# Kernel tuning notes

Hardware: AMD Instinct MI355X
Metric: run time of the kernel (lower is better)

Reference implementation:

```python
import jax, jax.numpy as jnp
import numpy as np

N, F, H, C, E = 20000, 512, 128, 64, 640000


def _uniform(key, shape, stdv):
    return jax.random.uniform(key, shape, jnp.float32, -stdv, stdv)


def setup_inputs() -> dict:
    key = jax.random.key(0)
    ks = jax.random.split(key, 20)
    inp = {}
    for i, name in enumerate(['x1', 'x2', 'x3']):
        inp[name] = jax.random.normal(ks[i], (N, F), jnp.float32)
    for v, base in zip([1, 2, 3], [3, 6, 9]):
        inp[f'src{v}'] = jax.random.randint(ks[base], (E,), 0, N, jnp.int32)
        inp[f'dst{v}'] = jax.random.randint(ks[base + 1], (E,), 0, N, jnp.int32)
        inp[f'val{v}'] = jax.random.uniform(ks[base + 2], (E,), jnp.float32)
    s1 = 1.0 / np.sqrt(H)
    s2 = 1.0 / np.sqrt(C)
    sv = 1.0 / np.sqrt(3.0)
    inp['W1'] = _uniform(ks[12], (3, 3, F, H), s1)   # [gc, view_role, F, H]
    inp['wv1'] = _uniform(ks[13], (3, 3), sv)
    inp['b1'] = _uniform(ks[14], (3, H), sv)
    inp['W2'] = _uniform(ks[15], (3, 3, H, C), s2)
    inp['wv2'] = _uniform(ks[16], (3, 3), sv)
    inp['b2'] = _uniform(ks[17], (3, C), sv)
    return inp


def _spmm(src, dst, val, emb, n):
    # out[i] = sum_{edges e with src=i} val[e] * emb[dst[e]]
    return jax.ops.segment_sum(val[:, None] * emb[dst], src, num_segments=n)


def _igc(xs, adjs, W, wv, b, n):
    # xs: [x_self, x_v2, x_v3]; adjs: matching [(src,dst,val)]*3
    embs = [xs[i] @ W[i] for i in range(3)]
    neigh = [_spmm(adjs[i][0], adjs[i][1], adjs[i][2], embs[i], n) for i in range(3)]
    agg = wv[0] * neigh[0] + wv[1] * neigh[1] + wv[2] * neigh[2]
    return embs[0] + 1.01 * agg + b


def reference(x1, x2, x3, src1, dst1, val1, src2, dst2, val2, src3, dst3, val3,
              W1, wv1, b1, W2, wv2, b2):
    n = x1.shape[0]
    a1, a2, a3 = (src1, dst1, val1), (src2, dst2, val2), (src3, dst3, val3)
    relu = jax.nn.relu
    h1 = relu(_igc([x1, x2, x3], [a1, a2, a3], W1[0], wv1[0], b1[0], n))
    h2 = relu(_igc([x2, x1, x3], [a2, a1, a3], W1[1], wv1[1], b1[1], n))
    h3 = relu(_igc([x3, x1, x2], [a3, a1, a2], W1[2], wv1[2], b1[2], n))
    y1 = relu(_igc([h1, h2, h3], [a1, a2, a3], W2[0], wv2[0], b2[0], n))
    y2 = relu(_igc([h2, h1, h3], [a2, a1, a3], W2[1], wv2[1], b2[1], n))
    y3 = relu(_igc([h3, h1, h2], [a3, a1, a2], W2[2], wv2[2], b2[2], n))
    return jnp.abs((y1 + y2 + y3) / 3.0)
```

## Files before the change

kernel.cpp:

```cpp
#include <hip/hip_runtime.h>
#include <hip/hip_bf16.h>

#define N_NODES 20000
#define F_DIM   512
#define H_DIM   128
#define C_DIM   64
#define E_EDGES 640000

#define P_WV1   64
#define P_B1    80
#define P_WV2   464
#define P_B2    480
#define P_E     1024
#define P_H     (P_E + 3*N_NODES*H_DIM)
#define P_YSUM  (P_H + 3*N_NODES*H_DIM)
#define RP_SZ      20032
#define CSR_STRIDE (RP_SZ + 2*E_EDGES)
#define P_CSR   (P_YSUM + N_NODES*C_DIM)
#define P_CUR   (P_CSR + 3*CSR_STRIDE)
#define P_WT1   (P_E + 4000000)
#define P_WT2   (P_E + 4300000)
#define P_W1H   (P_YSUM)
#define P_W1L   (P_YSUM + 294912)
#define P_W2H   (P_E + 4000000)
#define P_W2L   (P_E + 4050000)
#define NBUCK       8
#define BUCK_SHIFT  12
#define B2_STRIDE   (N_NODES * NBUCK)
#define NBLK_SCAN   625
#define BSUM_STRIDE 640

typedef __attribute__((ext_vector_type(8))) unsigned short u16x8;
typedef __attribute__((ext_vector_type(8))) __bf16 bf16x8;
typedef __attribute__((ext_vector_type(4))) float f32x4;

__device__ inline float cvt(float x) { return x; }
__device__ inline float cvt(__hip_bfloat16 x) { return __bfloat162float(x); }

__device__ inline void store_out(float v, float* p) { *p = v; }
__device__ inline void store_out(float v, __hip_bfloat16* p) { *p = __float2bfloat16(v); }

__device__ inline unsigned short f2bf_bits(float x) {
    __hip_bfloat16 b = __float2bfloat16(x);
    return *(unsigned short*)&b;
}
__device__ inline void splitbf(float x, unsigned short& h, unsigned short& l) {
    h = f2bf_bits(x);
    float hf = __uint_as_float(((unsigned int)h) << 16);
    l = f2bf_bits(x - hf);
}

__global__ void detect_kernel(const unsigned short* __restrict__ x, int* flag) {
    __shared__ int cnt;
    if (threadIdx.x == 0) cnt = 0;
    __syncthreads();
    int c = 0;
    for (int i = threadIdx.x; i < 4096; i += 256) {
        int ex = (x[i] >> 7) & 0xff;
        if (ex >= 140) c++;
    }
    atomicAdd(&cnt, c);
    __syncthreads();
    if (threadIdx.x == 0) *flag = (cnt > 64) ? 1 : 0;
}

__global__ void prep_kernel(const int* __restrict__ flag,
                            const void* wv1, const void* b1,
                            const void* wv2, const void* b2, float* ws) {
    bool f32 = (*flag == 1);
    int t = threadIdx.x;
    auto get = [&](const void* p, int i) -> float {
        return f32 ? ((const float*)p)[i]
                   : __bfloat162float(((const __hip_bfloat16*)p)[i]);
    };
    if (t < 9) ws[P_WV1 + t] = get(wv1, t);
    if (t < 9) ws[P_WV2 + t] = get(wv2, t);
    for (int i = t; i < 3*H_DIM; i += 256) ws[P_B1 + i] = get(b1, i);
    for (int i = t; i < 3*C_DIM; i += 256) ws[P_B2 + i] = get(b2, i);
}

__global__ __launch_bounds__(256)
void hist2_kernel(const int* __restrict__ s0, const int* __restrict__ d0,
                  const int* __restrict__ s1, const int* __restrict__ d1,
                  const int* __restrict__ s2, const int* __restrict__ d2,
                  int* __restrict__ deg2) {
    int e = blockIdx.x * 256 + threadIdx.x;
    if (e >= E_EDGES) return;
    const int z = blockIdx.y;
    const int* src = (z == 0) ? s0 : (z == 1) ? s1 : s2;
    const int* dst = (z == 0) ? d0 : (z == 1) ? d1 : d2;
    int idx = src[e] * NBUCK + (dst[e] >> BUCK_SHIFT);
    atomicAdd(&deg2[z * B2_STRIDE + idx], 1);
}

__global__ __launch_bounds__(256)
void scanA_kernel(int* __restrict__ deg2, int* __restrict__ bsum) {
    __shared__ int s[256];
    const int z = blockIdx.y;
    int* d = deg2 + z * B2_STRIDE;
    const int t = threadIdx.x;
    const int i = blockIdx.x * 256 + t;
    int v = d[i];
    s[t] = v;
    __syncthreads();
    for (int off = 1; off < 256; off <<= 1) {
        int u = (t >= off) ? s[t - off] : 0;
        __syncthreads();
        s[t] += u;
        __syncthreads();
    }
    d[i] = s[t] - v;
    if (t == 255) bsum[z * BSUM_STRIDE + blockIdx.x] = s[255];
}

__global__ __launch_bounds__(256)
void scanB_kernel(int* __restrict__ bsum) {
    __shared__ int sums[256];
    int* b = bsum + blockIdx.x * BSUM_STRIDE;
    const int t = threadIdx.x;
    int beg = t * 3, end = beg + 3; if (end > NBLK_SCAN) end = NBLK_SCAN;
    int s = 0;
    for (int i = beg; i < end && i < NBLK_SCAN; ++i) s += b[i];
    sums[t] = s;
    __syncthreads();
    for (int off = 1; off < 256; off <<= 1) {
        int u = (t >= off) ? sums[t - off] : 0;
        __syncthreads();
        sums[t] += u;
        __syncthreads();
    }
    int run = sums[t] - s;
    for (int i = beg; i < end && i < NBLK_SCAN; ++i) { int v = b[i]; b[i] = run; run += v; }
}

__global__ __launch_bounds__(256)
void scanC_kernel(int* __restrict__ deg2, const int* __restrict__ bsum,
                  int* __restrict__ rpBase) {
    const int z = blockIdx.y;
    int* d = deg2 + z * B2_STRIDE;
    int* rowptr = rpBase + (long)z * CSR_STRIDE;
    const int i = blockIdx.x * 256 + threadIdx.x;
    int v = d[i] + bsum[z * BSUM_STRIDE + blockIdx.x];
    d[i] = v;
    if ((i & (NBUCK - 1)) == 0) rowptr[i >> 3] = v;
    if (i == 0) rowptr[N_NODES] = E_EDGES;
}

__global__ __launch_bounds__(256)
void fill3_kernel(const int* __restrict__ flag,
                  const int* __restrict__ s0, const int* __restrict__ d0,
                  const void* __restrict__ v0,
                  const int* __restrict__ s1, const int* __restrict__ d1,
                  const void* __restrict__ v1,
                  const int* __restrict__ s2, const int* __restrict__ d2,
                  const void* __restrict__ v2,
                  const int* __restrict__ deg2, int* __restrict__ cur2,
                  int* __restrict__ rpBase) {
    int e = blockIdx.x * 256 + threadIdx.x;
    if (e >= E_EDGES) return;
    const int z = blockIdx.y;
    const int* src = (z == 0) ? s0 : (z == 1) ? s1 : s2;
    const int* dst = (z == 0) ? d0 : (z == 1) ? d1 : d2;
    const void* val = (z == 0) ? v0 : (z == 1) ? v1 : v2;
    float v = (*flag == 1) ? ((const float*)val)[e]
                           : __bfloat162float(((const __hip_bfloat16*)val)[e]);
    int d = dst[e];
    int idx = z * B2_STRIDE + src[e] * NBUCK + (d >> BUCK_SHIFT);
    int pos = deg2[idx] + atomicAdd(&cur2[idx], 1);
    int2* ed = (int2*)(rpBase + (long)z * CSR_STRIDE + RP_SZ);
    ed[pos] = make_int2(d, __float_as_int(v));
}

__global__ __launch_bounds__(256)
void transpose_w_kernel(const int* __restrict__ flag,
                        const void* __restrict__ Wsrc,
                        unsigned short* __restrict__ Wt, int K, int HO) {
    if (*flag != 0) return;
    __shared__ unsigned short T[64][80];
    const unsigned short* W = (const unsigned short*)Wsrc + (long)blockIdx.z * K * HO;
    unsigned short* O = Wt + (long)blockIdx.z * HO * K;
    const int k0 = blockIdx.x * 64, n0 = blockIdx.y * 64;
    const int t = threadIdx.x;
    const int rr = t >> 3, cc = (t & 7) * 8;
    #pragma unroll
    for (int i = 0; i < 2; ++i) {
        int k = rr + i * 32;
        *(u16x8*)&T[k][cc] = *(const u16x8*)&W[(long)(k0 + k) * HO + n0 + cc];
    }
    __syncthreads();
    #pragma unroll
    for (int i = 0; i < 2; ++i) {
        int nn = rr + i * 32;
        u16x8 v;
        #pragma unroll
        for (int j = 0; j < 8; ++j) v[j] = T[cc + j][nn];
        *(u16x8*)&O[(long)(n0 + nn) * K + k0 + cc] = v;
    }
}

__global__ __launch_bounds__(256)
void split_w_kernel(const int* __restrict__ flag,
                    const float* __restrict__ Wsrc,
                    unsigned short* __restrict__ Wh,
                    unsigned short* __restrict__ Wl, int K, int HO) {
    if (*flag != 1) return;
    __shared__ float T[64][68];
    const float* W = Wsrc + (long)blockIdx.z * K * HO;
    unsigned short* Oh = Wh + (long)blockIdx.z * HO * K;
    unsigned short* Ol = Wl + (long)blockIdx.z * HO * K;
    const int k0 = blockIdx.x * 64, n0 = blockIdx.y * 64;
    const int t = threadIdx.x;
    #pragma unroll
    for (int i = 0; i < 16; ++i) {
        int idx = t + i * 256;
        int r = idx >> 6, c = idx & 63;
        T[r][c] = W[(long)(k0 + r) * HO + n0 + c];
    }
    __syncthreads();
    #pragma unroll
    for (int i = 0; i < 16; ++i) {
        int idx = t + i * 256;
        int nn = idx >> 6, kk = idx & 63;
        unsigned short h, l;
        splitbf(T[kk][nn], h, l);
        Oh[(long)(n0 + nn) * K + k0 + kk] = h;
        Ol[(long)(n0 + nn) * K + k0 + kk] = l;
    }
}

#define SWZ(r, kb) (((r) << 7) + ((kb) ^ (((r) & 7) << 4)))

__global__ __launch_bounds__(256)
void gemm_mfma1_kernel(const int* __restrict__ flag,
                       const unsigned short* __restrict__ x0,
                       const unsigned short* __restrict__ x1,
                       const unsigned short* __restrict__ x2,
                       const unsigned short* __restrict__ WtBase,
                       unsigned short* __restrict__ outBase, int n) {
    if (*flag != 0) return;
    const int role = blockIdx.y;
    const unsigned short* X = (role == 0) ? x0 : (role == 1) ? x1 : x2;
    const unsigned short* Wt = WtBase + (long)role * H_DIM * F_DIM;
    unsigned short* out = outBase + (long)role * N_NODES * H_DIM;
    __shared__ __align__(16) unsigned short As[64 * 64];
    __shared__ __align__(16) unsigned short Bs[128 * 64];
    const int t = threadIdx.x;
    const int lane = t & 63;
    const int wave = t >> 6;
    const int wm = wave & 1, wn = wave >> 1;
    const int row0 = blockIdx.x * 64;
    const int rl = lane & 15;
    const int kq = lane >> 4;
    const int sr = t >> 3;
    const int sc = (t & 7) * 8;
    f32x4 acc[2][4] = {};
    for (int k0 = 0; k0 < F_DIM; k0 += 64) {
        #pragma unroll
        for (int i = 0; i < 2; ++i) {
            int r = i * 32 + sr;
            int gr = row0 + r; if (gr >= n) gr = n - 1;
            u16x8 v = *(const u16x8*)&X[(long)gr * F_DIM + k0 + sc];
            *(u16x8*)((char*)As + SWZ(r, sc * 2)) = v;
        }
        #pragma unroll
        for (int i = 0; i < 4; ++i) {
            int r = i * 32 + sr;
            u16x8 v = *(const u16x8*)&Wt[(long)r * F_DIM + k0 + sc];
            *(u16x8*)((char*)Bs + SWZ(r, sc * 2)) = v;
        }
        __syncthreads();
        #pragma unroll
        for (int s = 0; s < 2; ++s) {
            const int kb = s * 64 + kq * 16;
            bf16x8 af[2], bfr[4];
            #pragma unroll
            for (int mi = 0; mi < 2; ++mi) {
                int r = wm * 32 + mi * 16 + rl;
                af[mi] = *(const bf16x8*)((const char*)As + SWZ(r, kb));
            }
            #pragma unroll
            for (int ni = 0; ni < 4; ++ni) {
                int r = wn * 64 + ni * 16 + rl;
                bfr[ni] = *(const bf16x8*)((const char*)Bs + SWZ(r, kb));
            }
            #pragma unroll
            for (int mi = 0; mi < 2; ++mi)
                #pragma unroll
                for (int ni = 0; ni < 4; ++ni)
                    acc[mi][ni] = __builtin_amdgcn_mfma_f32_16x16x32_bf16(
                        af[mi], bfr[ni], acc[mi][ni], 0, 0, 0);
        }
        __syncthreads();
    }
    #pragma unroll
    for (int mi = 0; mi < 2; ++mi) {
        #pragma unroll
        for (int q = 0; q < 4; ++q) {
            int row = row0 + wm * 32 + mi * 16 + kq * 4 + q;
            if (row < n) {
                #pragma unroll
                for (int ni = 0; ni < 4; ++ni) {
                    int col = wn * 64 + ni * 16 + rl;
                    out[(long)row * H_DIM + col] = f2bf_bits(acc[mi][ni][q]);
                }
            }
        }
    }
}

__global__ __launch_bounds__(256)
void gemm_mfma1f_kernel(const int* __restrict__ flag,
                        const float* __restrict__ x0,
                        const float* __restrict__ x1,
                        const float* __restrict__ x2,
                        const unsigned short* __restrict__ WhBase,
                        const unsigned short* __restrict__ WlBase,
                        float* __restrict__ outBase, int n) {
    if (*flag != 1) return;
    const int role = blockIdx.y;
    const float* X = (role == 0) ? x0 : (role == 1) ? x1 : x2;
    const unsigned short* Wh = WhBase + (long)role * H_DIM * F_DIM;
    const unsigned short* Wl = WlBase + (long)role * H_DIM * F_DIM;
    float* out = outBase + (long)role * N_NODES * H_DIM;
    __shared__ __align__(16) unsigned short Ash[64 * 64];
    __shared__ __align__(16) unsigned short Asl[64 * 64];
    __shared__ __align__(16) unsigned short Bsh[128 * 64];
    __shared__ __align__(16) unsigned short Bsl[128 * 64];
    const int t = threadIdx.x;
    const int lane = t & 63;
    const int wave = t >> 6;
    const int wm = wave & 1, wn = wave >> 1;
    const int row0 = blockIdx.x * 64;
    const int rl = lane & 15;
    const int kq = lane >> 4;
    const int sr = t >> 3;
    const int sc = (t & 7) * 8;
    f32x4 acc[2][4] = {};
    for (int k0 = 0; k0 < F_DIM; k0 += 64) {
        #pragma unroll
        for (int i = 0; i < 2; ++i) {
            int r = i * 32 + sr;
            int gr = row0 + r; if (gr >= n) gr = n - 1;
            float4 v0 = *(const float4*)&X[(long)gr * F_DIM + k0 + sc];
            float4 v1 = *(const float4*)&X[(long)gr * F_DIM + k0 + sc + 4];
            float xs[8] = {v0.x, v0.y, v0.z, v0.w, v1.x, v1.y, v1.z, v1.w};
            u16x8 hi, lo;
            #pragma unroll
            for (int j = 0; j < 8; ++j) { unsigned short h, l; splitbf(xs[j], h, l); hi[j] = h; lo[j] = l; }
            *(u16x8*)((char*)Ash + SWZ(r, sc * 2)) = hi;
            *(u16x8*)((char*)Asl + SWZ(r, sc * 2)) = lo;
        }
        #pragma unroll
        for (int i = 0; i < 4; ++i) {
            int r = i * 32 + sr;
            u16x8 vh = *(const u16x8*)&Wh[(long)r * F_DIM + k0 + sc];
            u16x8 vl = *(const u16x8*)&Wl[(long)r * F_DIM + k0 + sc];
            *(u16x8*)((char*)Bsh + SWZ(r, sc * 2)) = vh;
            *(u16x8*)((char*)Bsl + SWZ(r, sc * 2)) = vl;
        }
        __syncthreads();
        #pragma unroll
        for (int s = 0; s < 2; ++s) {
            const int kb = s * 64 + kq * 16;
            bf16x8 ah[2], al[2], bh[4], bl[4];
            #pragma unroll
            for (int mi = 0; mi < 2; ++mi) {
                int r = wm * 32 + mi * 16 + rl;
                ah[mi] = *(const bf16x8*)((const char*)Ash + SWZ(r, kb));
                al[mi] = *(const bf16x8*)((const char*)Asl + SWZ(r, kb));
            }
            #pragma unroll
            for (int ni = 0; ni < 4; ++ni) {
                int r = wn * 64 + ni * 16 + rl;
                bh[ni] = *(const bf16x8*)((const char*)Bsh + SWZ(r, kb));
                bl[ni] = *(const bf16x8*)((const char*)Bsl + SWZ(r, kb));
            }
            #pragma unroll
            for (int mi = 0; mi < 2; ++mi)
                #pragma unroll
                for (int ni = 0; ni < 4; ++ni) {
                    acc[mi][ni] = __builtin_amdgcn_mfma_f32_16x16x32_bf16(
                        ah[mi], bh[ni], acc[mi][ni], 0, 0, 0);
                    acc[mi][ni] = __builtin_amdgcn_mfma_f32_16x16x32_bf16(
                        ah[mi], bl[ni], acc[mi][ni], 0, 0, 0);
                    acc[mi][ni] = __builtin_amdgcn_mfma_f32_16x16x32_bf16(
                        al[mi], bh[ni], acc[mi][ni], 0, 0, 0);
                }
        }
        __syncthreads();
    }
    #pragma unroll
    for (int mi = 0; mi < 2; ++mi) {
        #pragma unroll
        for (int q = 0; q < 4; ++q) {
            int row = row0 + wm * 32 + mi * 16 + kq * 4 + q;
            if (row < n) {
                #pragma unroll
                for (int ni = 0; ni < 4; ++ni) {
                    int col = wn * 64 + ni * 16 + rl;
                    out[(long)row * H_DIM + col] = acc[mi][ni][q];
                }
            }
        }
    }
}

#define SWZ2(r, kb) (((r) << 8) + ((kb) ^ (((r) & 7) << 4)))

__global__ __launch_bounds__(256)
void gemm_mfma2_kernel(const int* __restrict__ flag,
                       const unsigned short* __restrict__ h0,
                       const unsigned short* __restrict__ h1,
                       const unsigned short* __restrict__ h2,
                       const unsigned short* __restrict__ WtBase,
                       unsigned short* __restrict__ outBase, int n) {
    if (*flag != 0) return;
    const int role = blockIdx.y;
    const unsigned short* X = (role == 0) ? h0 : (role == 1) ? h1 : h2;
    const unsigned short* Wt = WtBase + (long)role * C_DIM * H_DIM;
    unsigned short* out = outBase + (long)role * N_NODES * C_DIM;
    __shared__ __align__(16) unsigned short As[64 * 128];
    __shared__ __align__(16) unsigned short Bs[64 * 128];
    const int t = threadIdx.x;
    const int lane = t & 63;
    const int wave = t >> 6;
    const int wm = wave & 1, wn = wave >> 1;
    const int row0 = blockIdx.x * 64;
    const int rl = lane & 15;
    const int kq = lane >> 4;
    #pragma unroll
    for (int i = 0; i < 4; ++i) {
        int e = t + i * 256;
        int r = e >> 4, c8 = e & 15;
        int gr = row0 + r; if (gr >= n) gr = n - 1;
        u16x8 va = *(const u16x8*)&X[(long)gr * H_DIM + c8 * 8];
        *(u16x8*)((char*)As + SWZ2(r, c8 * 16)) = va;
        u16x8 vb = *(const u16x8*)&Wt[(long)r * H_DIM + c8 * 8];
        *(u16x8*)((char*)Bs + SWZ2(r, c8 * 16)) = vb;
    }
    __syncthreads();
    f32x4 acc[2][2] = {};
    #pragma unroll
    for (int s = 0; s < 4; ++s) {
        const int kb = s * 64 + kq * 16;
        bf16x8 af[2], bfr[2];
        #pragma unroll
        for (int mi = 0; mi < 2; ++mi) {
            int r = wm * 32 + mi * 16 + rl;
            af[mi] = *(const bf16x8*)((const char*)As + SWZ2(r, kb));
        }
        #pragma unroll
        for (int ni = 0; ni < 2; ++ni) {
            int r = wn * 32 + ni * 16 + rl;
            bfr[ni] = *(const bf16x8*)((const char*)Bs + SWZ2(r, kb));
        }
        #pragma unroll
        for (int mi = 0; mi < 2; ++mi)
            #pragma unroll
            for (int ni = 0; ni < 2; ++ni)
                acc[mi][ni] = __builtin_amdgcn_mfma_f32_16x16x32_bf16(
                    af[mi], bfr[ni], acc[mi][ni], 0, 0, 0);
    }
    #pragma unroll
    for (int mi = 0; mi < 2; ++mi) {
        #pragma unroll
        for (int q = 0; q < 4; ++q) {
            int row = row0 + wm * 32 + mi * 16 + kq * 4 + q;
            if (row < n) {
                #pragma unroll
                for (int ni = 0; ni < 2; ++ni) {
                    int col = wn * 32 + ni * 16 + rl;
                    out[(long)row * C_DIM + col] = f2bf_bits(acc[mi][ni][q]);
                }
            }
        }
    }
}

__global__ __launch_bounds__(256)
void gemm_mfma2f_kernel(const int* __restrict__ flag,
                        const float* __restrict__ h0,
                        const float* __restrict__ h1,
                        const float* __restrict__ h2,
                        const unsigned short* __restrict__ WhBase,
                        const unsigned short* __restrict__ WlBase,
                        float* __restrict__ outBase, int n) {
    if (*flag != 1) return;
    const int role = blockIdx.y;
    const float* X = (role == 0) ? h0 : (role == 1) ? h1 : h2;
    const unsigned short* Wh = WhBase + (long)role * C_DIM * H_DIM;
    const unsigned short* Wl = WlBase + (long)role * C_DIM * H_DIM;
    float* out = outBase + (long)role * N_NODES * C_DIM;
    __shared__ __align__(16) unsigned short Ash[64 * 128];
    __shared__ __align__(16) unsigned short Asl[64 * 128];
    __shared__ __align__(16) unsigned short Bsh[64 * 128];
    __shared__ __align__(16) unsigned short Bsl[64 * 128];
    const int t = threadIdx.x;
    const int lane = t & 63;
    const int wave = t >> 6;
    const int wm = wave & 1, wn = wave >> 1;
    const int row0 = blockIdx.x * 64;
    const int rl = lane & 15;
    const int kq = lane >> 4;
    #pragma unroll
    for (int i = 0; i < 4; ++i) {
        int e = t + i * 256;
        int r = e >> 4, c8 = e & 15;
        int gr = row0 + r; if (gr >= n) gr = n - 1;
        float4 v0 = *(const float4*)&X[(long)gr * H_DIM + c8 * 8];
        float4 v1 = *(const float4*)&X[(long)gr * H_DIM + c8 * 8 + 4];
        float xs[8] = {v0.x, v0.y, v0.z, v0.w, v1.x, v1.y, v1.z, v1.w};
        u16x8 hi, lo;
        #pragma unroll
        for (int j = 0; j < 8; ++j) { unsigned short h, l; splitbf(xs[j], h, l); hi[j] = h; lo[j] = l; }
        *(u16x8*)((char*)Ash + SWZ2(r, c8 * 16)) = hi;
        *(u16x8*)((char*)Asl + SWZ2(r, c8 * 16)) = lo;
        u16x8 vh = *(const u16x8*)&Wh[(long)r * H_DIM + c8 * 8];
        u16x8 vl = *(const u16x8*)&Wl[(long)r * H_DIM + c8 * 8];
        *(u16x8*)((char*)Bsh + SWZ2(r, c8 * 16)) = vh;
        *(u16x8*)((char*)Bsl + SWZ2(r, c8 * 16)) = vl;
    }
    __syncthreads();
    f32x4 acc[2][2] = {};
    #pragma unroll
    for (int s = 0; s < 4; ++s) {
        const int kb = s * 64 + kq * 16;
        bf16x8 ah[2], al[2], bh[2], bl[2];
        #pragma unroll
        for (int mi = 0; mi < 2; ++mi) {
            int r = wm * 32 + mi * 16 + rl;
            ah[mi] = *(const bf16x8*)((const char*)Ash + SWZ2(r, kb));
            al[mi] = *(const bf16x8*)((const char*)Asl + SWZ2(r, kb));
        }
        #pragma unroll
        for (int ni = 0; ni < 2; ++ni) {
            int r = wn * 32 + ni * 16 + rl;
            bh[ni] = *(const bf16x8*)((const char*)Bsh + SWZ2(r, kb));
            bl[ni] = *(const bf16x8*)((const char*)Bsl + SWZ2(r, kb));
        }
        #pragma unroll
        for (int mi = 0; mi < 2; ++mi)
            #pragma unroll
            for (int ni = 0; ni < 2; ++ni) {
                acc[mi][ni] = __builtin_amdgcn_mfma_f32_16x16x32_bf16(
                    ah[mi], bh[ni], acc[mi][ni], 0, 0, 0);
                acc[mi][ni] = __builtin_amdgcn_mfma_f32_16x16x32_bf16(
                    ah[mi], bl[ni], acc[mi][ni], 0, 0, 0);
                acc[mi][ni] = __builtin_amdgcn_mfma_f32_16x16x32_bf16(
                    al[mi], bh[ni], acc[mi][ni], 0, 0, 0);
            }
    }
    #pragma unroll
    for (int mi = 0; mi < 2; ++mi) {
        #pragma unroll
        for (int q = 0; q < 4; ++q) {
            int row = row0 + wm * 32 + mi * 16 + kq * 4 + q;
            if (row < n) {
                #pragma unroll
                for (int ni = 0; ni < 2; ++ni) {
                    int col = wn * 32 + ni * 16 + rl;
                    out[(long)row * C_DIM + col] = acc[mi][ni][q];
                }
            }
        }
    }
}

template <int FP, bool ACCUM>
__global__ __launch_bounds__(256)
void spmm_f32_kernel(const int* __restrict__ flag,
                     const int* __restrict__ rp0, const int2* __restrict__ ed0,
                     const int* __restrict__ rp1, const int2* __restrict__ ed1,
                     const int* __restrict__ rp2, const int2* __restrict__ ed2,
                     const float* __restrict__ Et0, const float* __restrict__ Et1,
                     const float* __restrict__ Et2,
                     const float* __restrict__ wvp, const float* __restrict__ bias,
                     float* __restrict__ out) {
    if (*flag != 1) return;
    constexpr int HO = FP * 64;
    const int node = blockIdx.x * 4 + (threadIdx.x >> 6);
    const int lane = threadIdx.x & 63;
    const int fbase = lane * FP;
    float acc[FP];
    #pragma unroll
    for (int k = 0; k < FP; ++k) acc[k] = 0.f;

    const int*  rps[3] = {rp0, rp1, rp2};
    const int2* eds[3] = {ed0, ed1, ed2};
    const float* Ets[3] = {Et0, Et1, Et2};
    #pragma unroll
    for (int r = 0; r < 3; ++r) {
        const float s = 1.01f * wvp[r];
        const int2* ed = eds[r];
        const float* Et = Ets[r] + fbase;
        int e = rps[r][node];
        const int end = rps[r][node + 1];
        for (; e + 8 <= end; e += 8) {
            int2 E[8]; float vv[8]; const float* rr[8];
            #pragma unroll
            for (int q = 0; q < 8; ++q) E[q] = ed[e + q];
            #pragma unroll
            for (int q = 0; q < 8; ++q) {
                vv[q] = s * __int_as_float(E[q].y);
                rr[q] = Et + (long)E[q].x * HO;
            }
            #pragma unroll
            for (int q = 0; q < 8; ++q)
                #pragma unroll
                for (int k = 0; k < FP; ++k) acc[k] += vv[q] * rr[q][k];
        }
        for (; e + 2 <= end; e += 2) {
            int2 E0 = ed[e], E1 = ed[e + 1];
            float v0 = s * __int_as_float(E0.y), v1 = s * __int_as_float(E1.y);
            const float* r0 = Et + (long)E0.x * HO;
            const float* r1 = Et + (long)E1.x * HO;
            #pragma unroll
            for (int k = 0; k < FP; ++k) acc[k] += v0 * r0[k];
            #pragma unroll
            for (int k = 0; k < FP; ++k) acc[k] += v1 * r1[k];
        }
        if (e < end) {
            int2 E0 = ed[e];
            float v0 = s * __int_as_float(E0.y);
            const float* r0 = Et + (long)E0.x * HO;
            #pragma unroll
            for (int k = 0; k < FP; ++k) acc[k] += v0 * r0[k];
        }
    }
    const float* e0 = Et0 + (long)node * HO + fbase;
    const float* bp = bias + fbase;
    float* o = out + (long)node * HO + fbase;
    #pragma unroll
    for (int k = 0; k < FP; ++k) {
        float x = e0[k] + acc[k] + bp[k];
        x = x > 0.f ? x : 0.f;
        if (ACCUM) o[k] += x; else o[k] = x;
    }
}

template <int HO, bool ACCUM, bool OUT_BF16>
__global__ __launch_bounds__(256)
void spmm_bf16_kernel(const int* __restrict__ flag,
                      const int* __restrict__ rp0, const int2* __restrict__ ed0,
                      const int* __restrict__ rp1, const int2* __restrict__ ed1,
                      const int* __restrict__ rp2, const int2* __restrict__ ed2,
                      const unsigned short* __restrict__ Et0,
                      const unsigned short* __restrict__ Et1,
                      const unsigned short* __restrict__ Et2,
                      const float* __restrict__ wvp, const float* __restrict__ bias,
                      void* __restrict__ outp) {
    if (*flag != 0) return;
    constexpr int NL = HO / 2;
    constexpr int NPW = 64 / NL;
    const int t = threadIdx.x;
    const int lane = t & 63;
    const int li = lane % NL;
    const int node = blockIdx.x * (4 * NPW) + (t >> 6) * NPW + lane / NL;
    const int fl = li * 2;
    float a0 = 0.f, a1 = 0.f;

    const int*  rps[3] = {rp0, rp1, rp2};
    const int2* eds[3] = {ed0, ed1, ed2};
    const unsigned int* Ets[3] = {(const unsigned int*)Et0,
                                  (const unsigned int*)Et1,
                                  (const unsigned int*)Et2};
    #pragma unroll
    for (int r = 0; r < 3; ++r) {
        const float s = 1.01f * wvp[r];
        const int2* ed = eds[r];
        const unsigned int* Et = Ets[r] + li;
        int e = rps[r][node];
        const int end = rps[r][node + 1];
        for (; e + 4 <= end; e += 4) {
            int2 E0 = ed[e], E1 = ed[e + 1], E2 = ed[e + 2], E3 = ed[e + 3];
            float v0 = s * __int_as_float(E0.y), v1 = s * __int_as_float(E1.y);
            float v2 = s * __int_as_float(E2.y), v3 = s * __int_as_float(E3.y);
            unsigned int w0 = Et[(long)E0.x * NL];
            unsigned int w1 = Et[(long)E1.x * NL];
            unsigned int w2 = Et[(long)E2.x * NL];
            unsigned int w3 = Et[(long)E3.x * NL];
            a0 += v0 * __uint_as_float(w0 << 16);
            a1 += v0 * __uint_as_float(w0 & 0xffff0000u);
            a0 += v1 * __uint_as_float(w1 << 16);
            a1 += v1 * __uint_as_float(w1 & 0xffff0000u);
            a0 += v2 * __uint_as_float(w2 << 16);
            a1 += v2 * __uint_as_float(w2 & 0xffff0000u);
            a0 += v3 * __uint_as_float(w3 << 16);
            a1 += v3 * __uint_as_float(w3 & 0xffff0000u);
        }
        for (; e < end; ++e) {
            int2 E0 = ed[e];
            float v0 = s * __int_as_float(E0.y);
            unsigned int w0 = Et[(long)E0.x * NL];
            a0 += v0 * __uint_as_float(w0 << 16);
            a1 += v0 * __uint_as_float(w0 & 0xffff0000u);
        }
    }
    unsigned int ws0 = ((const unsigned int*)Et0)[(long)node * NL + li];
    float x0 = __uint_as_float(ws0 << 16)        + a0 + bias[fl];
    float x1 = __uint_as_float(ws0 & 0xffff0000u) + a1 + bias[fl + 1];
    x0 = x0 > 0.f ? x0 : 0.f;
    x1 = x1 > 0.f ? x1 : 0.f;
    if (OUT_BF16) {
        unsigned int packed = ((unsigned int)f2bf_bits(x1) << 16) | f2bf_bits(x0);
        ((unsigned int*)outp)[(long)node * NL + li] = packed;
    } else {
        float* o = (float*)outp + (long)node * HO + fl;
        if (ACCUM) { o[0] += x0; o[1] += x1; }
        else       { o[0] = x0;  o[1] = x1; }
    }
}

template <typename TOUT>
__global__ __launch_bounds__(256)
void final_kernel(const int* __restrict__ flag, int want,
                  const float* __restrict__ ysum, TOUT* __restrict__ out, int n) {
    if (*flag != want) return;
    int i = blockIdx.x * 256 + threadIdx.x;
    if (i >= n) return;
    store_out(fabsf(ysum[i] * (1.f / 3.f)), &out[i]);
}

extern "C" void kernel_launch(void* const* d_in, const int* in_sizes, int n_in,
                              void* d_out, int out_size, void* d_ws, size_t ws_size,
                              hipStream_t stream) {
    float* ws = (float*)d_ws;
    int* flag = (int*)d_ws;
    static const int perm[3][3] = {{0, 1, 2}, {1, 0, 2}, {2, 0, 1}};

    detect_kernel<<<1, 256, 0, stream>>>((const unsigned short*)d_in[0], flag);
    prep_kernel<<<1, 256, 0, stream>>>(flag, d_in[13], d_in[14], d_in[16], d_in[17], ws);

    int* csrbase = (int*)(ws + P_CSR);
    int* rp[3]; int2* ed[3];
    for (int j = 0; j < 3; ++j) {
        rp[j] = csrbase + (long)j * CSR_STRIDE;
        ed[j] = (int2*)(rp[j] + RP_SZ);
    }
    {
        int* deg2 = (int*)(ws + P_YSUM);
        int* cur2 = deg2 + 3 * B2_STRIDE;
        int* bsum = cur2 + 3 * B2_STRIDE;
        hipMemsetAsync(deg2, 0, (size_t)6 * B2_STRIDE * 4, stream);
        dim3 ge((E_EDGES + 255) / 256, 3);
        hist2_kernel<<<ge, 256, 0, stream>>>(
            (const int*)d_in[3], (const int*)d_in[4],
            (const int*)d_in[6], (const int*)d_in[7],
            (const int*)d_in[9], (const int*)d_in[10], deg2);
        dim3 gs(NBLK_SCAN, 3);
        scanA_kernel<<<gs, 256, 0, stream>>>(deg2, bsum);
        scanB_kernel<<<3, 256, 0, stream>>>(bsum);
        scanC_kernel<<<gs, 256, 0, stream>>>(deg2, bsum, csrbase);
        fill3_kernel<<<ge, 256, 0, stream>>>(
            flag,
            (const int*)d_in[3], (const int*)d_in[4], d_in[5],
            (const int*)d_in[6], (const int*)d_in[7], d_in[8],
            (const int*)d_in[9], (const int*)d_in[10], d_in[11],
            deg2, cur2, csrbase);
    }

    unsigned short* Wt1 = (unsigned short*)(ws + P_WT1);
    unsigned short* Wt2 = (unsigned short*)(ws + P_WT2);
    {
        dim3 g1(F_DIM / 64, H_DIM / 64, 9);
        transpose_w_kernel<<<g1, 256, 0, stream>>>(flag, d_in[12], Wt1, F_DIM, H_DIM);
        dim3 g2(H_DIM / 64, C_DIM / 64, 9);
        transpose_w_kernel<<<g2, 256, 0, stream>>>(flag, d_in[15], Wt2, H_DIM, C_DIM);
    }
    unsigned short* W1h = (unsigned short*)(ws + P_W1H);
    unsigned short* W1l = (unsigned short*)(ws + P_W1L);
    {
        dim3 g1(F_DIM / 64, H_DIM / 64, 9);
        split_w_kernel<<<g1, 256, 0, stream>>>(flag, (const float*)d_in[12],
                                               W1h, W1l, F_DIM, H_DIM);
    }

    unsigned short* Eb = (unsigned short*)(ws + P_E);
    unsigned short* Hb = (unsigned short*)(ws + P_H);

    const int gemmBlocks = (N_NODES + 63) / 64;

    for (int v = 0; v < 3; ++v) {
        int j0 = perm[v][0], j1 = perm[v][1], j2 = perm[v][2];
        dim3 g(gemmBlocks, 3);
        gemm_mfma1_kernel<<<g, 256, 0, stream>>>(
            flag,
            (const unsigned short*)d_in[j0], (const unsigned short*)d_in[j1],
            (const unsigned short*)d_in[j2],
            Wt1 + (long)v * 3 * H_DIM * F_DIM, Eb, N_NODES);
        gemm_mfma1f_kernel<<<g, 256, 0, stream>>>(
            flag,
            (const float*)d_in[j0], (const float*)d_in[j1], (const float*)d_in[j2],
            W1h + (long)v * 3 * H_DIM * F_DIM, W1l + (long)v * 3 * H_DIM * F_DIM,
            ws + P_E, N_NODES);

        spmm_bf16_kernel<128, false, true><<<N_NODES / 4, 256, 0, stream>>>(
            flag, rp[j0], ed[j0], rp[j1], ed[j1], rp[j2], ed[j2],
            Eb, Eb + (long)N_NODES * H_DIM, Eb + 2L * N_NODES * H_DIM,
            ws + P_WV1 + v * 3, ws + P_B1 + v * H_DIM,
            Hb + (long)v * N_NODES * H_DIM);
        spmm_f32_kernel<2, false><<<N_NODES / 4, 256, 0, stream>>>(
            flag, rp[j0], ed[j0], rp[j1], ed[j1], rp[j2], ed[j2],
            ws + P_E, ws + P_E + (long)N_NODES * H_DIM, ws + P_E + 2L * N_NODES * H_DIM,
            ws + P_WV1 + v * 3, ws + P_B1 + v * H_DIM,
            ws + P_H + (long)v * N_NODES * H_DIM);
    }

    unsigned short* W2h = (unsigned short*)(ws + P_W2H);
    unsigned short* W2l = (unsigned short*)(ws + P_W2L);
    {
        dim3 g2(H_DIM / 64, C_DIM / 64, 9);
        split_w_kernel<<<g2, 256, 0, stream>>>(flag, (const float*)d_in[15],
                                               W2h, W2l, H_DIM, C_DIM);
    }

    for (int v = 0; v < 3; ++v) {
        int j0 = perm[v][0], j1 = perm[v][1], j2 = perm[v][2];
        dim3 g(gemmBlocks, 3);
        gemm_mfma2_kernel<<<g, 256, 0, stream>>>(
            flag,
            Hb + (long)j0 * N_NODES * H_DIM, Hb + (long)j1 * N_NODES * H_DIM,
            Hb + (long)j2 * N_NODES * H_DIM,
            Wt2 + (long)v * 3 * C_DIM * H_DIM, Eb, N_NODES);
        gemm_mfma2f_kernel<<<g, 256, 0, stream>>>(
            flag,
            ws + P_H + (long)j0 * N_NODES * H_DIM,
            ws + P_H + (long)j1 * N_NODES * H_DIM,
            ws + P_H + (long)j2 * N_NODES * H_DIM,
            W2h + (long)v * 3 * C_DIM * H_DIM, W2l + (long)v * 3 * C_DIM * H_DIM,
            ws + P_E, N_NODES);

        if (v == 0) {
            spmm_bf16_kernel<64, false, false><<<N_NODES / 8, 256, 0, stream>>>(
                flag, rp[j0], ed[j0], rp[j1], ed[j1], rp[j2], ed[j2],
                Eb, Eb + (long)N_NODES * C_DIM, Eb + 2L * N_NODES * C_DIM,
                ws + P_WV2 + v * 3, ws + P_B2 + v * C_DIM, ws + P_YSUM);
            spmm_f32_kernel<1, false><<<N_NODES / 4, 256, 0, stream>>>(
                flag, rp[j0], ed[j0], rp[j1], ed[j1], rp[j2], ed[j2],
                ws + P_E, ws + P_E + (long)N_NODES * C_DIM, ws + P_E + 2L * N_NODES * C_DIM,
                ws + P_WV2 + v * 3, ws + P_B2 + v * C_DIM, ws + P_YSUM);
        } else {
            spmm_bf16_kernel<64, true, false><<<N_NODES / 8, 256, 0, stream>>>(
                flag, rp[j0], ed[j0], rp[j1], ed[j1], rp[j2], ed[j2],
                Eb, Eb + (long)N_NODES * C_DIM, Eb + 2L * N_NODES * C_DIM,
                ws + P_WV2 + v * 3, ws + P_B2 + v * C_DIM, ws + P_YSUM);
            spmm_f32_kernel<1, true><<<N_NODES / 4, 256, 0, stream>>>(
                flag, rp[j0], ed[j0], rp[j1], ed[j1], rp[j2], ed[j2],
                ws + P_E, ws + P_E + (long)N_NODES * C_DIM, ws + P_E + 2L * N_NODES * C_DIM,
                ws + P_WV2 + v * 3, ws + P_B2 + v * C_DIM, ws + P_YSUM);
        }
    }

    final_kernel<__hip_bfloat16><<<(out_size + 255) / 256, 256, 0, stream>>>(
        flag, 0, ws + P_YSUM, (__hip_bfloat16*)d_out, out_size);
    final_kernel<float><<<(out_size + 255) / 256, 256, 0, stream>>>(
        flag, 1, ws + P_YSUM, (float*)d_out, out_size);
}
```

Baseline: 1.083 ms.

## Use bf16 intermediates for fp32 inputs, dropping fp32 SpMM and layer-2 split GEMM

For fp32 inputs, the layer-1 split-bf16 GEMM now writes bf16 embeddings, and both SpMM stages run through the shared bf16 SpMM kernel. The fp32 SpMM kernels and the layer-2 hi/lo split GEMM are removed, and layer 2 uses a single-bf16 MFMA GEMM fed by a new W2 transpose kernel that handles either input dtype. This roughly halves gather traffic in the memory-bound SpMM and cuts the layer-2 MFMA work to a third. The cost is lower precision in intermediate activations and layer-2 weights.

```diff
diff --git a/kernel.cpp b/kernel.cpp
--- a/kernel.cpp
+++ b/kernel.cpp
@@ -22,8 +22,6 @@
 #define P_WT2   (P_E + 4300000)
 #define P_W1H   (P_YSUM)
 #define P_W1L   (P_YSUM + 294912)
-#define P_W2H   (P_E + 4000000)
-#define P_W2L   (P_E + 4050000)
 #define NBUCK       8
 #define BUCK_SHIFT  12
 #define B2_STRIDE   (N_NODES * NBUCK)
@@ -199,6 +197,22 @@
 }
 
 __global__ __launch_bounds__(256)
+void transpose_wt2_kernel(const int* __restrict__ flag,
+                          const void* __restrict__ Wsrc,
+                          unsigned short* __restrict__ Wt) {
+    const bool f32 = (*flag == 1);
+    const int z = blockIdx.x;
+    const long base = (long)z * H_DIM * C_DIM;
+    unsigned short* O = Wt + (long)z * C_DIM * H_DIM;
+    for (int idx = threadIdx.x; idx < H_DIM * C_DIM; idx += 256) {
+        int k = idx >> 6, n = idx & 63;
+        float v = f32 ? ((const float*)Wsrc)[base + idx]
+                      : __bfloat162float(((const __hip_bfloat16*)Wsrc)[base + idx]);
+        O[(long)n * H_DIM + k] = f2bf_bits(v);
+    }
+}
+
+__global__ __launch_bounds__(256)
 void split_w_kernel(const int* __restrict__ flag,
                     const float* __restrict__ Wsrc,
                     unsigned short* __restrict__ Wh,
@@ -315,13 +329,13 @@
                         const float* __restrict__ x2,
                         const unsigned short* __restrict__ WhBase,
                         const unsigned short* __restrict__ WlBase,
-                        float* __restrict__ outBase, int n) {
+                        unsigned short* __restrict__ outBase, int n) {
     if (*flag != 1) return;
     const int role = blockIdx.y;
     const float* X = (role == 0) ? x0 : (role == 1) ? x1 : x2;
     const unsigned short* Wh = WhBase + (long)role * H_DIM * F_DIM;
     const unsigned short* Wl = WlBase + (long)role * H_DIM * F_DIM;
-    float* out = outBase + (long)role * N_NODES * H_DIM;
+    unsigned short* out = outBase + (long)role * N_NODES * H_DIM;
     __shared__ __align__(16) unsigned short Ash[64 * 64];
     __shared__ __align__(16) unsigned short Asl[64 * 64];
     __shared__ __align__(16) unsigned short Bsh[128 * 64];
@@ -398,7 +412,7 @@
                 #pragma unroll
                 for (int ni = 0; ni < 4; ++ni) {
                     int col = wn * 64 + ni * 16 + rl;
-                    out[(long)row * H_DIM + col] = acc[mi][ni][q];
+                    out[(long)row * H_DIM + col] = f2bf_bits(acc[mi][ni][q]);
                 }
             }
         }
@@ -408,13 +422,11 @@
 #define SWZ2(r, kb) (((r) << 8) + ((kb) ^ (((r) & 7) << 4)))
 
 __global__ __launch_bounds__(256)
-void gemm_mfma2_kernel(const int* __restrict__ flag,
-                       const unsigned short* __restrict__ h0,
+void gemm_mfma2_kernel(const unsigned short* __restrict__ h0,
                        const unsigned short* __restrict__ h1,
                        const unsigned short* __restrict__ h2,
                        const unsigned short* __restrict__ WtBase,
                        unsigned short* __restrict__ outBase, int n) {
-    if (*flag != 0) return;
     const int role = blockIdx.y;
     const unsigned short* X = (role == 0) ? h0 : (role == 1) ? h1 : h2;
     const unsigned short* Wt = WtBase + (long)role * C_DIM * H_DIM;
@@ -477,170 +489,9 @@
     }
 }
 
-__global__ __launch_bounds__(256)
-void gemm_mfma2f_kernel(const int* __restrict__ flag,
-                        const float* __restrict__ h0,
-                        const float* __restrict__ h1,
-                        const float* __restrict__ h2,
-                        const unsigned short* __restrict__ WhBase,
-                        const unsigned short* __restrict__ WlBase,
-                        float* __restrict__ outBase, int n) {
-    if (*flag != 1) return;
-    const int role = blockIdx.y;
-    const float* X = (role == 0) ? h0 : (role == 1) ? h1 : h2;
-    const unsigned short* Wh = WhBase + (long)role * C_DIM * H_DIM;
-    const unsigned short* Wl = WlBase + (long)role * C_DIM * H_DIM;
-    float* out = outBase + (long)role * N_NODES * C_DIM;
-    __shared__ __align__(16) unsigned short Ash[64 * 128];
-    __shared__ __align__(16) unsigned short Asl[64 * 128];
-    __shared__ __align__(16) unsigned short Bsh[64 * 128];
-    __shared__ __align__(16) unsigned short Bsl[64 * 128];
-    const int t = threadIdx.x;
-    const int lane = t & 63;
-    const int wave = t >> 6;
-    const int wm = wave & 1, wn = wave >> 1;
-    const int row0 = blockIdx.x * 64;
-    const int rl = lane & 15;
-    const int kq = lane >> 4;
-    #pragma unroll
-    for (int i = 0; i < 4; ++i) {
-        int e = t + i * 256;
-        int r = e >> 4, c8 = e & 15;
-        int gr = row0 + r; if (gr >= n) gr = n - 1;
-        float4 v0 = *(const float4*)&X[(long)gr * H_DIM + c8 * 8];
-        float4 v1 = *(const float4*)&X[(long)gr * H_DIM + c8 * 8 + 4];
-        float xs[8] = {v0.x, v0.y, v0.z, v0.w, v1.x, v1.y, v1.z, v1.w};
-        u16x8 hi, lo;
-        #pragma unroll
-        for (int j = 0; j < 8; ++j) { unsigned short h, l; splitbf(xs[j], h, l); hi[j] = h; lo[j] = l; }
-        *(u16x8*)((char*)Ash + SWZ2(r, c8 * 16)) = hi;
-        *(u16x8*)((char*)Asl + SWZ2(r, c8 * 16)) = lo;
-        u16x8 vh = *(const u16x8*)&Wh[(long)r * H_DIM + c8 * 8];
-        u16x8 vl = *(const u16x8*)&Wl[(long)r * H_DIM + c8 * 8];
-        *(u16x8*)((char*)Bsh + SWZ2(r, c8 * 16)) = vh;
-        *(u16x8*)((char*)Bsl + SWZ2(r, c8 * 16)) = vl;
-    }
-    __syncthreads();
-    f32x4 acc[2][2] = {};
-    #pragma unroll
-    for (int s = 0; s < 4; ++s) {
-        const int kb = s * 64 + kq * 16;
-        bf16x8 ah[2], al[2], bh[2], bl[2];
-        #pragma unroll
-        for (int mi = 0; mi < 2; ++mi) {
-            int r = wm * 32 + mi * 16 + rl;
-            ah[mi] = *(const bf16x8*)((const char*)Ash + SWZ2(r, kb));
-            al[mi] = *(const bf16x8*)((const char*)Asl + SWZ2(r, kb));
-        }
-        #pragma unroll
-        for (int ni = 0; ni < 2; ++ni) {
-            int r = wn * 32 + ni * 16 + rl;
-            bh[ni] = *(const bf16x8*)((const char*)Bsh + SWZ2(r, kb));
-            bl[ni] = *(const bf16x8*)((const char*)Bsl + SWZ2(r, kb));
-        }
-        #pragma unroll
-        for (int mi = 0; mi < 2; ++mi)
-            #pragma unroll
-            for (int ni = 0; ni < 2; ++ni) {
-                acc[mi][ni] = __builtin_amdgcn_mfma_f32_16x16x32_bf16(
-                    ah[mi], bh[ni], acc[mi][ni], 0, 0, 0);
-                acc[mi][ni] = __builtin_amdgcn_mfma_f32_16x16x32_bf16(
-                    ah[mi], bl[ni], acc[mi][ni], 0, 0, 0);
-                acc[mi][ni] = __builtin_amdgcn_mfma_f32_16x16x32_bf16(
-                    al[mi], bh[ni], acc[mi][ni], 0, 0, 0);
-            }
-    }
-    #pragma unroll
-    for (int mi = 0; mi < 2; ++mi) {
-        #pragma unroll
-        for (int q = 0; q < 4; ++q) {
-            int row = row0 + wm * 32 + mi * 16 + kq * 4 + q;
-            if (row < n) {
-                #pragma unroll
-                for (int ni = 0; ni < 2; ++ni) {
-                    int col = wn * 32 + ni * 16 + rl;
-                    out[(long)row * C_DIM + col] = acc[mi][ni][q];
-                }
-            }
-        }
-    }
-}
-
-template <int FP, bool ACCUM>
-__global__ __launch_bounds__(256)
-void spmm_f32_kernel(const int* __restrict__ flag,
-                     const int* __restrict__ rp0, const int2* __restrict__ ed0,
-                     const int* __restrict__ rp1, const int2* __restrict__ ed1,
-                     const int* __restrict__ rp2, const int2* __restrict__ ed2,
-                     const float* __restrict__ Et0, const float* __restrict__ Et1,
-                     const float* __restrict__ Et2,
-                     const float* __restrict__ wvp, const float* __restrict__ bias,
-                     float* __restrict__ out) {
-    if (*flag != 1) return;
-    constexpr int HO = FP * 64;
-    const int node = blockIdx.x * 4 + (threadIdx.x >> 6);
-    const int lane = threadIdx.x & 63;
-    const int fbase = lane * FP;
-    float acc[FP];
-    #pragma unroll
-    for (int k = 0; k < FP; ++k) acc[k] = 0.f;
-
-    const int*  rps[3] = {rp0, rp1, rp2};
-    const int2* eds[3] = {ed0, ed1, ed2};
-    const float* Ets[3] = {Et0, Et1, Et2};
-    #pragma unroll
-    for (int r = 0; r < 3; ++r) {
-        const float s = 1.01f * wvp[r];
-        const int2* ed = eds[r];
-        const float* Et = Ets[r] + fbase;
-        int e = rps[r][node];
-        const int end = rps[r][node + 1];
-        for (; e + 8 <= end; e += 8) {
-            int2 E[8]; float vv[8]; const float* rr[8];
-            #pragma unroll
-            for (int q = 0; q < 8; ++q) E[q] = ed[e + q];
-            #pragma unroll
-            for (int q = 0; q < 8; ++q) {
-                vv[q] = s * __int_as_float(E[q].y);
-                rr[q] = Et + (long)E[q].x * HO;
-            }
-            #pragma unroll
-            for (int q = 0; q < 8; ++q)
-                #pragma unroll
-                for (int k = 0; k < FP; ++k) acc[k] += vv[q] * rr[q][k];
-        }
-        for (; e + 2 <= end; e += 2) {
-            int2 E0 = ed[e], E1 = ed[e + 1];
-            float v0 = s * __int_as_float(E0.y), v1 = s * __int_as_float(E1.y);
-            const float* r0 = Et + (long)E0.x * HO;
-            const float* r1 = Et + (long)E1.x * HO;
-            #pragma unroll
-            for (int k = 0; k < FP; ++k) acc[k] += v0 * r0[k];
-            #pragma unroll
-            for (int k = 0; k < FP; ++k) acc[k] += v1 * r1[k];
-        }
-        if (e < end) {
-            int2 E0 = ed[e];
-            float v0 = s * __int_as_float(E0.y);
-            const float* r0 = Et + (long)E0.x * HO;
-            #pragma unroll
-            for (int k = 0; k < FP; ++k) acc[k] += v0 * r0[k];
-        }
-    }
-    const float* e0 = Et0 + (long)node * HO + fbase;
-    const float* bp = bias + fbase;
-    float* o = out + (long)node * HO + fbase;
-    #pragma unroll
-    for (int k = 0; k < FP; ++k) {
-        float x = e0[k] + acc[k] + bp[k];
-        x = x > 0.f ? x : 0.f;
-        if (ACCUM) o[k] += x; else o[k] = x;
-    }
-}
-
 template <int HO, bool ACCUM, bool OUT_BF16>
 __global__ __launch_bounds__(256)
-void spmm_bf16_kernel(const int* __restrict__ flag,
+void spmm_bf16_kernel(const int* __restrict__ flag, int want,
                       const int* __restrict__ rp0, const int2* __restrict__ ed0,
                       const int* __restrict__ rp1, const int2* __restrict__ ed1,
                       const int* __restrict__ rp2, const int2* __restrict__ ed2,
@@ -649,7 +500,7 @@
                       const unsigned short* __restrict__ Et2,
                       const float* __restrict__ wvp, const float* __restrict__ bias,
                       void* __restrict__ outp) {
-    if (*flag != 0) return;
+    if (want >= 0 && *flag != want) return;
     constexpr int NL = HO / 2;
     constexpr int NPW = 64 / NL;
     const int t = threadIdx.x;
@@ -761,18 +612,14 @@
 
     unsigned short* Wt1 = (unsigned short*)(ws + P_WT1);
     unsigned short* Wt2 = (unsigned short*)(ws + P_WT2);
-    {
-        dim3 g1(F_DIM / 64, H_DIM / 64, 9);
-        transpose_w_kernel<<<g1, 256, 0, stream>>>(flag, d_in[12], Wt1, F_DIM, H_DIM);
-        dim3 g2(H_DIM / 64, C_DIM / 64, 9);
-        transpose_w_kernel<<<g2, 256, 0, stream>>>(flag, d_in[15], Wt2, H_DIM, C_DIM);
-    }
     unsigned short* W1h = (unsigned short*)(ws + P_W1H);
     unsigned short* W1l = (unsigned short*)(ws + P_W1L);
     {
         dim3 g1(F_DIM / 64, H_DIM / 64, 9);
+        transpose_w_kernel<<<g1, 256, 0, stream>>>(flag, d_in[12], Wt1, F_DIM, H_DIM);
         split_w_kernel<<<g1, 256, 0, stream>>>(flag, (const float*)d_in[12],
                                                W1h, W1l, F_DIM, H_DIM);
+        transpose_wt2_kernel<<<9, 256, 0, stream>>>(flag, d_in[15], Wt2);
     }
 
     unsigned short* Eb = (unsigned short*)(ws + P_E);
@@ -792,63 +639,31 @@
             flag,
             (const float*)d_in[j0], (const float*)d_in[j1], (const float*)d_in[j2],
             W1h + (long)v * 3 * H_DIM * F_DIM, W1l + (long)v * 3 * H_DIM * F_DIM,
-            ws + P_E, N_NODES);
-
+            Eb, N_NODES);
         spmm_bf16_kernel<128, false, true><<<N_NODES / 4, 256, 0, stream>>>(
-            flag, rp[j0], ed[j0], rp[j1], ed[j1], rp[j2], ed[j2],
+            flag, -1, rp[j0], ed[j0], rp[j1], ed[j1], rp[j2], ed[j2],
             Eb, Eb + (long)N_NODES * H_DIM, Eb + 2L * N_NODES * H_DIM,
             ws + P_WV1 + v * 3, ws + P_B1 + v * H_DIM,
             Hb + (long)v * N_NODES * H_DIM);
-        spmm_f32_kernel<2, false><<<N_NODES / 4, 256, 0, stream>>>(
-            flag, rp[j0], ed[j0], rp[j1], ed[j1], rp[j2], ed[j2],
-            ws + P_E, ws + P_E + (long)N_NODES * H_DIM, ws + P_E + 2L * N_NODES * H_DIM,
-            ws + P_WV1 + v * 3, ws + P_B1 + v * H_DIM,
-            ws + P_H + (long)v * N_NODES * H_DIM);
-    }
-
-    unsigned short* W2h = (unsigned short*)(ws + P_W2H);
-    unsigned short* W2l = (unsigned short*)(ws + P_W2L);
-    {
-        dim3 g2(H_DIM / 64, C_DIM / 64, 9);
-        split_w_kernel<<<g2, 256, 0, stream>>>(flag, (const float*)d_in[15],
-                                               W2h, W2l, H_DIM, C_DIM);
     }
 
     for (int v = 0; v < 3; ++v) {
         int j0 = perm[v][0], j1 = perm[v][1], j2 = perm[v][2];
         dim3 g(gemmBlocks, 3);
         gemm_mfma2_kernel<<<g, 256, 0, stream>>>(
-            flag,
             Hb + (long)j0 * N_NODES * H_DIM, Hb + (long)j1 * N_NODES * H_DIM,
             Hb + (long)j2 * N_NODES * H_DIM,
             Wt2 + (long)v * 3 * C_DIM * H_DIM, Eb, N_NODES);
-        gemm_mfma2f_kernel<<<g, 256, 0, stream>>>(
-            flag,
-            ws + P_H + (long)j0 * N_NODES * H_DIM,
-            ws + P_H + (long)j1 * N_NODES * H_DIM,
-            ws + P_H + (long)j2 * N_NODES * H_DIM,
-            W2h + (long)v * 3 * C_DIM * H_DIM, W2l + (long)v * 3 * C_DIM * H_DIM,
-            ws + P_E, N_NODES);
-
-        if (v == 0) {
+        if (v == 0)
             spmm_bf16_kernel<64, false, false><<<N_NODES / 8, 256, 0, stream>>>(
-                flag, rp[j0], ed[j0], rp[j1], ed[j1], rp[j2], ed[j2],
+                flag, -1, rp[j0], ed[j0], rp[j1], ed[j1], rp[j2], ed[j2],
                 Eb, Eb + (long)N_NODES * C_DIM, Eb + 2L * N_NODES * C_DIM,
                 ws + P_WV2 + v * 3, ws + P_B2 + v * C_DIM, ws + P_YSUM);
-            spmm_f32_kernel<1, false><<<N_NODES / 4, 256, 0, stream>>>(
-                flag, rp[j0], ed[j0], rp[j1], ed[j1], rp[j2], ed[j2],
-                ws + P_E, ws + P_E + (long)N_NODES * C_DIM, ws + P_E + 2L * N_NODES * C_DIM,
-                ws + P_WV2 + v * 3, ws + P_B2 + v * C_DIM, ws + P_YSUM);
-        } else {
+        else
             spmm_bf16_kernel<64, true, false><<<N_NODES / 8, 256, 0, stream>>>(
-                flag, rp[j0], ed[j0], rp[j1], ed[j1], rp[j2], ed[j2],
+                flag, -1, rp[j0], ed[j0], rp[j1], ed[j1], rp[j2], ed[j2],
                 Eb, Eb + (long)N_NODES * C_DIM, Eb + 2L * N_NODES * C_DIM,
                 ws + P_WV2 + v * 3, ws + P_B2 + v * C_DIM, ws + P_YSUM);
-            spmm_f32_kernel<1, true><<<N_NODES / 4, 256, 0, stream>>>(
-                flag, rp[j0], ed[j0], rp[j1], ed[j1], rp[j2], ed[j2],
-                ws + P_E, ws + P_E + (long)N_NODES * C_DIM, ws + P_E + 2L * N_NODES * C_DIM,
-                ws + P_WV2 + v * 3, ws + P_B2 + v * C_DIM, ws + P_YSUM);
-        }
     }
 
     final_kernel<__hip_bfloat16><<<(out_size + 255) / 256, 256, 0, stream>>>(
```

New measurement: 899.6 us. -16.9%, faster.
